# Kernel optimization log

Hardware: AMD Instinct MI355X
Metric: run time of the kernel (lower is better)

The kernel has to match this reference:

```python
import jax, jax.numpy as jnp
import numpy as np

FACTOR = 2
DIM = 3
F3 = FACTOR ** DIM  # 8 children per voxel
N = 1_000_000
C = 64
K = 4  # exactly K active children per voxel -> static output size M = N*K


def setup_inputs() -> dict:
    key = jax.random.key(0)
    k1, k2, k3 = jax.random.split(key, 3)
    coords = jax.random.randint(k1, (N, DIM + 1), 0, 512, dtype=jnp.int32)
    feats = jax.random.normal(k2, (N, C), dtype=jnp.float32)
    # binary subdivision mask with exactly K ones per row (static nonzero count)
    r = jax.random.uniform(k3, (N, F3))
    rank = jnp.argsort(jnp.argsort(r, axis=-1), axis=-1)
    sub = (rank < K).astype(jnp.int32)
    return {"feats": feats, "coords": coords, "sub": sub}


def reference(feats, coords, sub):
    n = coords.shape[0]
    M = n * K  # static total number of output voxels
    # flat nonzero indices over [N*F3]; sorted, equivalent to torch's
    # row-major nonzero() + repeat_interleave index construction
    flat = jnp.nonzero(sub.reshape(-1), size=M, fill_value=0)[0]
    idx = flat // F3      # parent voxel index (== repeat_interleave(arange(N), N_leaf))
    subidx = flat % F3    # child slot within the 2x2x2 cell
    # new_coords: scale spatial coords by factor, add per-child octant offset
    scale = jnp.array([1] + [FACTOR] * DIM, dtype=coords.dtype)
    off = jnp.stack(
        [jnp.zeros_like(subidx)] + [(subidx // FACTOR**i) % FACTOR for i in range(DIM)],
        axis=1,
    ).astype(coords.dtype)
    new_coords = (coords * scale)[idx] + off  # [M, 1+DIM]
    # channel -> spatial: reshape feats to [N*F3, C/F3], gather child features
    x_feats = feats.reshape(n * F3, C // F3)
    new_feats = x_feats[idx * F3 + subidx]  # == x_feats[flat], [M, C/F3]
    return new_feats, new_coords
```

## Files before the change

### kernel.cpp

```cpp
#include <hip/hip_runtime.h>
#include <hip/hip_bf16.h>


__global__ __launch_bounds__(256) void sc2s_kernel(
    const float* __restrict__ feats,
    const int*   __restrict__ coords,
    const int*   __restrict__ sub,
    float* __restrict__ out_feats,
    float* __restrict__ out_coords,
    int M) {
  int r = blockIdx.x * blockDim.x + threadIdx.x;
  if (r >= M) return;
  int i = r >> 2;
  int k = r & 3;

  const int4* s4 = reinterpret_cast<const int4*>(sub) + (size_t)i * 2;
  int4 a = s4[0];
  int4 b = s4[1];
  unsigned m = (unsigned)(a.x != 0)
             | ((unsigned)(a.y != 0) << 1)
             | ((unsigned)(a.z != 0) << 2)
             | ((unsigned)(a.w != 0) << 3)
             | ((unsigned)(b.x != 0) << 4)
             | ((unsigned)(b.y != 0) << 5)
             | ((unsigned)(b.z != 0) << 6)
             | ((unsigned)(b.w != 0) << 7);
  #pragma unroll
  for (int t = 0; t < 3; ++t) {
    if (t < k) m &= (m - 1);
  }
  int j = __ffs(m) - 1;

  const float4* f4 = reinterpret_cast<const float4*>(feats) + (size_t)i * 16 + (size_t)j * 2;
  float4 f0 = f4[0];
  float4 f1 = f4[1];
  float4* of = reinterpret_cast<float4*>(out_feats) + (size_t)r * 2;
  of[0] = f0;
  of[1] = f1;

  int4 c = reinterpret_cast<const int4*>(coords)[i];
  float4 oc;
  oc.x = (float)c.x;
  oc.y = (float)(c.y * 2 + (j & 1));
  oc.z = (float)(c.z * 2 + ((j >> 1) & 1));
  oc.w = (float)(c.w * 2 + ((j >> 2) & 1));
  reinterpret_cast<float4*>(out_coords)[r] = oc;
}

extern "C" void kernel_launch(void* const* d_in, const int* in_sizes, int n_in,
                              void* d_out, int out_size, void* d_ws, size_t ws_size,
                              hipStream_t stream) {
  const float* feats  = (const float*)d_in[0];
  const int*   coords = (const int*)d_in[1];
  const int*   sub    = (const int*)d_in[2];

  int M = out_size / 12;
  float* out_feats  = (float*)d_out;
  float* out_coords = (float*)d_out + (size_t)M * 8;

  int block = 256;
  int grid = (M + block - 1) / block;
  sc2s_kernel<<<grid, block, 0, stream>>>(feats, coords, sub, out_feats, out_coords, M);
}
```

Before: 91.75 us.

## Split work into one float4 per thread and use nontemporal stores

Each thread now writes exactly one 16-byte output vector, so consecutive threads write consecutive addresses across both the feature and coordinate regions, making stores fully coalesced. Previously each thread wrote two adjacent float4s plus a separate coords float4. Output stores now use nontemporal hints to avoid polluting cache. The cost is three times as many threads and redundant reloads of the mask, bit selection and parent data across threads.

Measured after the change: 85.68 us. -6.6%, faster.

```diff
diff --git a/kernel.cpp b/kernel.cpp
--- a/kernel.cpp
+++ b/kernel.cpp
@@ -2,21 +2,10 @@
 #include <hip/hip_bf16.h>
 
 
-__global__ __launch_bounds__(256) void sc2s_kernel(
-    const float* __restrict__ feats,
-    const int*   __restrict__ coords,
-    const int*   __restrict__ sub,
-    float* __restrict__ out_feats,
-    float* __restrict__ out_coords,
-    int M) {
-  int r = blockIdx.x * blockDim.x + threadIdx.x;
-  if (r >= M) return;
-  int i = r >> 2;
-  int k = r & 3;
+typedef float f4 __attribute__((ext_vector_type(4)));
+typedef int   i4 __attribute__((ext_vector_type(4)));
 
-  const int4* s4 = reinterpret_cast<const int4*>(sub) + (size_t)i * 2;
-  int4 a = s4[0];
-  int4 b = s4[1];
+__device__ __forceinline__ int kth_set_bit(const i4& a, const i4& b, int k) {
   unsigned m = (unsigned)(a.x != 0)
              | ((unsigned)(a.y != 0) << 1)
              | ((unsigned)(a.z != 0) << 2)
@@ -26,25 +15,46 @@
              | ((unsigned)(b.z != 0) << 6)
              | ((unsigned)(b.w != 0) << 7);
   #pragma unroll
-  for (int t = 0; t < 3; ++t) {
-    if (t < k) m &= (m - 1);
+  for (int q = 0; q < 3; ++q) {
+    if (q < k) m &= (m - 1);
   }
-  int j = __ffs(m) - 1;
+  return __ffs(m) - 1;
+}
 
-  const float4* f4 = reinterpret_cast<const float4*>(feats) + (size_t)i * 16 + (size_t)j * 2;
-  float4 f0 = f4[0];
-  float4 f1 = f4[1];
-  float4* of = reinterpret_cast<float4*>(out_feats) + (size_t)r * 2;
-  of[0] = f0;
-  of[1] = f1;
+__global__ __launch_bounds__(256) void sc2s_kernel(
+    const float* __restrict__ feats,
+    const int*   __restrict__ coords,
+    const int*   __restrict__ sub,
+    float*       __restrict__ out,
+    int M) {
+  int t = blockIdx.x * blockDim.x + threadIdx.x;
+  if (t >= 3 * M) return;
 
-  int4 c = reinterpret_cast<const int4*>(coords)[i];
-  float4 oc;
-  oc.x = (float)c.x;
-  oc.y = (float)(c.y * 2 + (j & 1));
-  oc.z = (float)(c.z * 2 + ((j >> 1) & 1));
-  oc.w = (float)(c.w * 2 + ((j >> 2) & 1));
-  reinterpret_cast<float4*>(out_coords)[r] = oc;
+  if (t < 2 * M) {
+    int r    = t >> 1;
+    int half = t & 1;
+    int i    = r >> 2;
+    int k    = r & 3;
+    const i4* s4 = reinterpret_cast<const i4*>(sub) + (size_t)i * 2;
+    i4 a = s4[0], b = s4[1];
+    int j = kth_set_bit(a, b, k);
+    f4 v = reinterpret_cast<const f4*>(feats)[(size_t)i * 16 + j * 2 + half];
+    __builtin_nontemporal_store(v, reinterpret_cast<f4*>(out) + t);
+  } else {
+    int r = t - 2 * M;
+    int i = r >> 2;
+    int k = r & 3;
+    const i4* s4 = reinterpret_cast<const i4*>(sub) + (size_t)i * 2;
+    i4 a = s4[0], b = s4[1];
+    int j = kth_set_bit(a, b, k);
+    i4 c = reinterpret_cast<const i4*>(coords)[i];
+    f4 o;
+    o.x = (float)c.x;
+    o.y = (float)(c.y * 2 + (j & 1));
+    o.z = (float)(c.z * 2 + ((j >> 1) & 1));
+    o.w = (float)(c.w * 2 + ((j >> 2) & 1));
+    __builtin_nontemporal_store(o, reinterpret_cast<f4*>(out) + t);
+  }
 }
 
 extern "C" void kernel_launch(void* const* d_in, const int* in_sizes, int n_in,
@@ -55,10 +65,8 @@
   const int*   sub    = (const int*)d_in[2];
 
   int M = out_size / 12;
-  float* out_feats  = (float*)d_out;
-  float* out_coords = (float*)d_out + (size_t)M * 8;
-
+  int total = 3 * M;
   int block = 256;
-  int grid = (M + block - 1) / block;
-  sc2s_kernel<<<grid, block, 0, stream>>>(feats, coords, sub, out_feats, out_coords, M);
+  int grid = (total + block - 1) / block;
+  sc2s_kernel<<<grid, block, 0, stream>>>(feats, coords, sub, (float*)d_out, M);
 }
```

## Stage voxel features in LDS per block and emit outputs with coalesced nontemporal stores

Applied to the files above, without the earlier changes.

Each block now owns 64 parent voxels instead of 256 output rows. It loads their full feature rows, masks and coords into shared memory with coalesced vector loads, and decodes each subdivision mask once per voxel rather than once per child. The outputs are then written with fully coalesced nontemporal stores. This targets scattered partial-row reads and redundant mask loads, at the cost of LDS use and a block barrier. It also drops the tail bounds check, so it relies on N being a multiple of 64.

Result: faster. 80.84 us, median of 2 (-11.9%).

```diff
diff --git a/kernel.cpp b/kernel.cpp
--- a/kernel.cpp
+++ b/kernel.cpp
@@ -1,50 +1,81 @@
 #include <hip/hip_runtime.h>
 #include <hip/hip_bf16.h>
 
+
+typedef float f4 __attribute__((ext_vector_type(4)));
+typedef int   i4 __attribute__((ext_vector_type(4)));
+
+#define VPB 64
+#define ROWP 68
 
 __global__ __launch_bounds__(256) void sc2s_kernel(
     const float* __restrict__ feats,
     const int*   __restrict__ coords,
     const int*   __restrict__ sub,
-    float* __restrict__ out_feats,
-    float* __restrict__ out_coords,
-    int M) {
-  int r = blockIdx.x * blockDim.x + threadIdx.x;
-  if (r >= M) return;
-  int i = r >> 2;
-  int k = r & 3;
+    float*       __restrict__ out_feats,
+    float*       __restrict__ out_coords,
+    int N) {
+  __shared__ __align__(16) float sf[VPB * ROWP];
+  __shared__ int sj[VPB];
+  __shared__ __align__(16) int sc[VPB * 4];
 
-  const int4* s4 = reinterpret_cast<const int4*>(sub) + (size_t)i * 2;
-  int4 a = s4[0];
-  int4 b = s4[1];
-  unsigned m = (unsigned)(a.x != 0)
-             | ((unsigned)(a.y != 0) << 1)
-             | ((unsigned)(a.z != 0) << 2)
-             | ((unsigned)(a.w != 0) << 3)
-             | ((unsigned)(b.x != 0) << 4)
-             | ((unsigned)(b.y != 0) << 5)
-             | ((unsigned)(b.z != 0) << 6)
-             | ((unsigned)(b.w != 0) << 7);
+  int b   = blockIdx.x;
+  int tid = threadIdx.x;
+  int v0  = b * VPB;
+
+  {
+    int vi = tid >> 2, w0 = (tid & 3) << 4;
+    const f4* src = reinterpret_cast<const f4*>(feats + (size_t)(v0 + vi) * 64 + w0);
+    f4* dst = reinterpret_cast<f4*>(&sf[vi * ROWP + w0]);
+    #pragma unroll
+    for (int q = 0; q < 4; ++q) dst[q] = src[q];
+  }
+  if (tid < VPB) {
+    const i4* s4 = reinterpret_cast<const i4*>(sub) + (size_t)(v0 + tid) * 2;
+    i4 a = s4[0], bb = s4[1];
+    unsigned m = (unsigned)(a.x != 0)
+               | ((unsigned)(a.y != 0) << 1)
+               | ((unsigned)(a.z != 0) << 2)
+               | ((unsigned)(a.w != 0) << 3)
+               | ((unsigned)(bb.x != 0) << 4)
+               | ((unsigned)(bb.y != 0) << 5)
+               | ((unsigned)(bb.z != 0) << 6)
+               | ((unsigned)(bb.w != 0) << 7);
+    int j0 = __ffs(m) - 1; m &= m - 1;
+    int j1 = __ffs(m) - 1; m &= m - 1;
+    int j2 = __ffs(m) - 1; m &= m - 1;
+    int j3 = __ffs(m) - 1;
+    sj[tid] = j0 | (j1 << 8) | (j2 << 16) | (j3 << 24);
+  } else if (tid < 2 * VPB) {
+    int vi = tid - VPB;
+    reinterpret_cast<i4*>(sc)[vi] = reinterpret_cast<const i4*>(coords)[v0 + vi];
+  }
+  __syncthreads();
+
+  f4* ofb = reinterpret_cast<f4*>(out_feats) + (size_t)b * (VPB * 8);
   #pragma unroll
-  for (int t = 0; t < 3; ++t) {
-    if (t < k) m &= (m - 1);
+  for (int p = 0; p < 2; ++p) {
+    int cc   = tid + p * 256;
+    int vi   = cc >> 3;
+    int k    = (cc >> 1) & 3;
+    int half = cc & 1;
+    int j    = (sj[vi] >> (k * 8)) & 0xff;
+    f4 v = *reinterpret_cast<const f4*>(&sf[vi * ROWP + j * 8 + half * 4]);
+    __builtin_nontemporal_store(v, ofb + cc);
   }
-  int j = __ffs(m) - 1;
-
-  const float4* f4 = reinterpret_cast<const float4*>(feats) + (size_t)i * 16 + (size_t)j * 2;
-  float4 f0 = f4[0];
-  float4 f1 = f4[1];
-  float4* of = reinterpret_cast<float4*>(out_feats) + (size_t)r * 2;
-  of[0] = f0;
-  of[1] = f1;
-
-  int4 c = reinterpret_cast<const int4*>(coords)[i];
-  float4 oc;
-  oc.x = (float)c.x;
-  oc.y = (float)(c.y * 2 + (j & 1));
-  oc.z = (float)(c.z * 2 + ((j >> 1) & 1));
-  oc.w = (float)(c.w * 2 + ((j >> 2) & 1));
-  reinterpret_cast<float4*>(out_coords)[r] = oc;
+  {
+    int cc = tid;
+    int vi = cc >> 2;
+    int k  = cc & 3;
+    int j  = (sj[vi] >> (k * 8)) & 0xff;
+    const int* c = &sc[vi * 4];
+    f4 o;
+    o.x = (float)c[0];
+    o.y = (float)(c[1] * 2 + (j & 1));
+    o.z = (float)(c[2] * 2 + ((j >> 1) & 1));
+    o.w = (float)(c[3] * 2 + ((j >> 2) & 1));
+    __builtin_nontemporal_store(o, reinterpret_cast<f4*>(out_coords) + (size_t)b * (VPB * 4) + cc);
+  }
 }
 
 extern "C" void kernel_launch(void* const* d_in, const int* in_sizes, int n_in,
@@ -55,10 +86,10 @@
   const int*   sub    = (const int*)d_in[2];
 
   int M = out_size / 12;
+  int N = M / 4;
   float* out_feats  = (float*)d_out;
   float* out_coords = (float*)d_out + (size_t)M * 8;
 
-  int block = 256;
-  int grid = (M + block - 1) / block;
-  sc2s_kernel<<<grid, block, 0, stream>>>(feats, coords, sub, out_feats, out_coords, M);
+  int grid = (N + VPB - 1) / VPB;
+  sc2s_kernel<<<grid, 256, 0, stream>>>(feats, coords, sub, out_feats, out_coords, N);
 }
```
